# Kernel optimization log

Hardware: AMD Instinct MI355X
Metric: run time of the kernel (lower is better)

The kernel has to match this reference:

```python
import jax, jax.numpy as jnp
import numpy as np

N = 50000        # num_nodes
R = 51           # num_relations
B = 12           # num_bases (hard-coded in module)
D_IN = 64        # initial_size
D_MID = 64       # middle_size
D_OUT2 = 128     # output_size - middle_size - initial_size = 256 - 64 - 64
E = 1600000      # num edges (avg degree 32)


def setup_inputs() -> dict:
    key = jax.random.key(0)
    ks = jax.random.split(key, 11)
    return {
        "edge_index": jax.random.randint(ks[0], (2, E), 0, N),
        "edge_type": jax.random.randint(ks[1], (E,), 0, R),
        "emb": jax.random.normal(ks[2], (N, D_IN)) * 0.1,
        "basis1": jax.random.normal(ks[3], (B, D_IN, D_MID)) * 0.05,
        "comp1": jax.random.normal(ks[4], (R, B)) * 0.3,
        "root1": jax.random.normal(ks[5], (D_IN, D_MID)) * 0.05,
        "bias1": jnp.zeros((D_MID,), jnp.float32),
        "basis2": jax.random.normal(ks[6], (B, D_MID, D_OUT2)) * 0.05,
        "comp2": jax.random.normal(ks[7], (R, B)) * 0.3,
        "root2": jax.random.normal(ks[8], (D_MID, D_OUT2)) * 0.05,
        "bias2": jnp.zeros((D_OUT2,), jnp.float32),
    }


def _rgcn_conv(x, edge_index, edge_type, basis, comp, root, bias):
    """PyG RGCNConv with basis decomposition, per-relation MEAN aggregation,
    root weight and bias. Uses the exact identity
      mean_e(x[src_e] @ W_r) = (mean_e x[src_e]) @ W_r
    to aggregate first (per (node, relation) segment), then transform.
    """
    num_nodes, d_in = x.shape
    src, dst = edge_index[0], edge_index[1]
    seg = dst * R + edge_type                      # combined (node, relation) id
    x_src = x[src]                                 # [E, d_in] gather
    sums = jax.ops.segment_sum(x_src, seg, num_segments=num_nodes * R)
    cnt = jax.ops.segment_sum(jnp.ones((src.shape[0],), x.dtype), seg,
                              num_segments=num_nodes * R)
    agg = (sums / jnp.maximum(cnt, 1.0)[:, None]).reshape(num_nodes, R, d_in)
    W = jnp.einsum('rb,bio->rio', comp, basis)     # [R, d_in, d_out]
    out = jnp.einsum('nri,rio->no', agg, W)        # sum over relations
    return out + x @ root + bias


def reference(edge_index, edge_type, emb, basis1, comp1, root1, bias1,
              basis2, comp2, root2, bias2):
    x1 = jax.nn.relu(_rgcn_conv(emb, edge_index, edge_type, basis1, comp1, root1, bias1))
    x2 = jax.nn.relu(_rgcn_conv(x1, edge_index, edge_type, basis2, comp2, root2, bias2))
    # dropout(p=0.2) is identity in eval mode
    return jnp.concatenate([x2, x1, emb], axis=1)  # [N, 256]
```

## Files before the change

kernel.cpp:

```cpp
#include <hip/hip_runtime.h>
#include <hip/hip_bf16.h>

#define R_REL 51
#define N_BASE 12

typedef __attribute__((ext_vector_type(8))) unsigned short u16x8;
typedef __attribute__((ext_vector_type(8))) short bf16x8;
typedef __attribute__((ext_vector_type(4))) float f32x4;

__device__ __forceinline__ float bf2f(unsigned short u) {
  union { unsigned int i; float f; } c; c.i = ((unsigned int)u) << 16; return c.f;
}
__device__ __forceinline__ unsigned short f2bf(float f) {
  union { float f; unsigned int i; } c; c.f = f;
  return (unsigned short)((c.i + 0x7FFFu + ((c.i >> 16) & 1u)) >> 16);
}

__global__ void k_count(const int* __restrict__ dst, int* __restrict__ cnt, int E) {
  int i = blockIdx.x * 256 + threadIdx.x;
  if (i < E) atomicAdd(&cnt[dst[i]], 1);
}

__global__ void k_scan1(const int* __restrict__ cnt, int* __restrict__ rowptr,
                        int* __restrict__ bsums, int n) {
  __shared__ int s[256];
  int tid = threadIdx.x;
  int i = blockIdx.x * 256 + tid;
  int v = (i < n) ? cnt[i] : 0;
  s[tid] = v;
  __syncthreads();
  for (int off = 1; off < 256; off <<= 1) {
    int t = (tid >= off) ? s[tid - off] : 0;
    __syncthreads();
    s[tid] += t;
    __syncthreads();
  }
  if (i < n) rowptr[i] = s[tid] - v;
  if (tid == 255) bsums[blockIdx.x] = s[255];
}

__global__ void k_scan2(int* __restrict__ bsums, int nb) {
  __shared__ int s[256];
  int tid = threadIdx.x;
  int v = (tid < nb) ? bsums[tid] : 0;
  s[tid] = v;
  __syncthreads();
  for (int off = 1; off < 256; off <<= 1) {
    int t = (tid >= off) ? s[tid - off] : 0;
    __syncthreads();
    s[tid] += t;
    __syncthreads();
  }
  if (tid < nb) bsums[tid] = s[tid] - v;
}

__global__ void k_scan3(int* __restrict__ rowptr, const int* __restrict__ bsums,
                        int n, int E) {
  int i = blockIdx.x * 256 + threadIdx.x;
  if (i < n) rowptr[i] += bsums[blockIdx.x];
  if (blockIdx.x == 0 && threadIdx.x == 0) rowptr[n] = E;
}

__global__ void k_scatter(const int* __restrict__ src, const int* __restrict__ dst,
                          const int* __restrict__ typ, const int* __restrict__ rowptr,
                          int* __restrict__ cursor, unsigned int* __restrict__ edges, int E) {
  int i = blockIdx.x * 256 + threadIdx.x;
  if (i < E) {
    int d = dst[i];
    int pos = rowptr[d] + atomicAdd(&cursor[d], 1);
    edges[pos] = (unsigned int)src[i] | ((unsigned int)typ[i] << 16);
  }
}

__global__ __launch_bounds__(256) void k_agg(
    const float* __restrict__ x,
    int xstride,
    const int* __restrict__ rowptr,
    const unsigned int* __restrict__ edges,
    const float* __restrict__ comp,
    unsigned short* __restrict__ Z,
    int n0, int n1) {
  __shared__ float comp_lds[R_REL * N_BASE];
  __shared__ int   hist[4][64];
  __shared__ float inv[4][64];
  int tid = threadIdx.x;
  for (int idx = tid; idx < R_REL * N_BASE; idx += 256) comp_lds[idx] = comp[idx];
  int wid = tid >> 6, lane = tid & 63;
  if (lane < R_REL) hist[wid][lane] = 0;
  __syncthreads();

  int n = n0 + blockIdx.x * 4 + wid;
  bool valid = (n < n1);
  int e0 = 0, e1 = 0;
  if (valid) { e0 = rowptr[n]; e1 = rowptr[n + 1]; }
  e0 = __builtin_amdgcn_readfirstlane(e0);
  e1 = __builtin_amdgcn_readfirstlane(e1);

  for (int j = e0 + lane; j < e1; j += 64)
    atomicAdd(&hist[wid][edges[j] >> 16], 1);
  __syncthreads();
  if (lane < R_REL) {
    int c = hist[wid][lane];
    inv[wid][lane] = (c > 0) ? (1.0f / (float)c) : 0.0f;
  }
  __syncthreads();

  float z[N_BASE];
#pragma unroll
  for (int b = 0; b < N_BASE; b++) z[b] = 0.0f;

  int j = e0;
  for (; j + 2 <= e1; j += 2) {
    unsigned int eA = edges[j], eB = edges[j + 1];
    int sA = eA & 0xFFFF, rA = eA >> 16;
    int sB = eB & 0xFFFF, rB = eB >> 16;
    float xA = x[(size_t)sA * xstride + lane];
    float xB = x[(size_t)sB * xstride + lane];
    float tA = xA * inv[wid][rA];
    float tB = xB * inv[wid][rB];
    const float* cA = &comp_lds[rA * N_BASE];
    const float* cB = &comp_lds[rB * N_BASE];
#pragma unroll
    for (int b = 0; b < N_BASE; b++) z[b] += tA * cA[b] + tB * cB[b];
  }
  if (j < e1) {
    unsigned int eA = edges[j];
    int sA = eA & 0xFFFF, rA = eA >> 16;
    float xA = x[(size_t)sA * xstride + lane];
    float tA = xA * inv[wid][rA];
    const float* cA = &comp_lds[rA * N_BASE];
#pragma unroll
    for (int b = 0; b < N_BASE; b++) z[b] += tA * cA[b];
  }

  if (valid) {
    size_t base = (size_t)(n - n0) * 832;
#pragma unroll
    for (int b = 0; b < N_BASE; b++)
      Z[base + b * 64 + lane] = f2bf(z[b]);
    Z[base + 768 + lane] = f2bf(x[(size_t)n * xstride + lane]);
  }
}

template <int NOUT>
__global__ void k_prep_w(const float* __restrict__ basis, const float* __restrict__ root,
                         unsigned short* __restrict__ Wf, int total) {
  int idx = blockIdx.x * 256 + threadIdx.x;
  if (idx >= total) return;
  constexpr int NT = NOUT / 16;
  int j = idx & 7;
  int l = (idx >> 3) & 63;
  int t = idx >> 9;
  int nt = t % NT, ks = t / NT;
  int k = ks * 32 + ((l >> 4) * 8) + j;
  int col = nt * 16 + (l & 15);
  float v = (k < 768) ? basis[(size_t)k * NOUT + col]
                      : root[(size_t)(k - 768) * NOUT + col];
  Wf[idx] = f2bf(v);
}

template <int NOUT>
__global__ __launch_bounds__(256) void k_gemm_mfma(
    const unsigned short* __restrict__ Z,
    const unsigned short* __restrict__ Wf,
    const float* __restrict__ bias,
    float* __restrict__ dout,
    int col_off, int n0, int n1) {
  constexpr int NT = NOUT / 16;
  int tid = threadIdx.x;
  int w = tid >> 6, l = tid & 63;
  int m0 = n0 + blockIdx.x * 64 + w * 16;
  int arow = m0 + (l & 15);
  if (arow > n1 - 1) arow = n1 - 1;
  const unsigned short* zp = Z + (size_t)(arow - n0) * 832 + ((l >> 4) * 8);
  const unsigned short* wp = Wf + (size_t)l * 8;

  f32x4 acc[NT];
#pragma unroll
  for (int t = 0; t < NT; t++) acc[t] = (f32x4){0.0f, 0.0f, 0.0f, 0.0f};

  for (int ks = 0; ks < 26; ks++) {
    bf16x8 a = *(const bf16x8*)(zp + ks * 32);
#pragma unroll
    for (int nt = 0; nt < NT; nt++) {
      bf16x8 b = *(const bf16x8*)(wp + (size_t)(ks * NT + nt) * 512);
      acc[nt] = __builtin_amdgcn_mfma_f32_16x16x32_bf16(a, b, acc[nt], 0, 0, 0);
    }
  }

  int rbase = m0 + ((l >> 4) * 4);
  int cl = l & 15;
#pragma unroll
  for (int nt = 0; nt < NT; nt++) {
    int col = col_off + nt * 16 + cl;
    float bv = bias[nt * 16 + cl];
#pragma unroll
    for (int j = 0; j < 4; j++) {
      int row = rbase + j;
      if (row < n1)
        dout[(size_t)row * 256 + col] = fmaxf(acc[nt][j] + bv, 0.0f);
    }
  }
}

__global__ void k_copy_emb(const float* __restrict__ emb, float* __restrict__ dout, int n) {
  int i = blockIdx.x * 256 + threadIdx.x;
  int row = i >> 4, c4 = i & 15;
  if (row < n) {
    float4 v = ((const float4*)emb)[(size_t)row * 16 + c4];
    ((float4*)dout)[(size_t)row * 64 + 48 + c4] = v;
  }
}

extern "C" void kernel_launch(void* const* d_in, const int* in_sizes, int n_in,
                              void* d_out, int out_size, void* d_ws, size_t ws_size,
                              hipStream_t stream) {
  const int*   edge_index = (const int*)d_in[0];
  const int*   edge_type  = (const int*)d_in[1];
  const float* emb        = (const float*)d_in[2];
  const float* basis1     = (const float*)d_in[3];
  const float* comp1      = (const float*)d_in[4];
  const float* root1      = (const float*)d_in[5];
  const float* bias1      = (const float*)d_in[6];
  const float* basis2     = (const float*)d_in[7];
  const float* comp2      = (const float*)d_in[8];
  const float* root2      = (const float*)d_in[9];
  const float* bias2      = (const float*)d_in[10];

  int E = in_sizes[1];
  int N = in_sizes[2] / 64;
  const int* srcp = edge_index;
  const int* dstp = edge_index + E;

  char* ws = (char*)d_ws;
  size_t o = 0;
  auto take = [&](size_t bytes) -> char* {
    char* p = ws + o;
    o += (bytes + 255) & ~(size_t)255;
    return p;
  };
  int*  cnt    = (int*)take((size_t)N * 4);
  int*  rowptr = (int*)take((size_t)(N + 1) * 4);
  int*  bsums  = (int*)take(4096);
  int*  cursor = (int*)take((size_t)N * 4);
  size_t zero_bytes = o;
  unsigned int* edges = (unsigned int*)take((size_t)E * 4);
  constexpr int W1_ELEMS = 26 * 4 * 512;
  constexpr int W2_ELEMS = 26 * 8 * 512;
  unsigned short* Wf1 = (unsigned short*)take((size_t)W1_ELEMS * 2);
  unsigned short* Wf2 = (unsigned short*)take((size_t)W2_ELEMS * 2);
  size_t fixed_end = o;

  size_t avail = (ws_size > fixed_end) ? (ws_size - fixed_end) : 0;
  long long nc = (long long)(avail / (832 * 2));
  if (nc > N) nc = N;
  int nchunk = (int)(nc & ~63LL);
  if (nchunk < 64) nchunk = 64;
  unsigned short* Zb = (unsigned short*)(ws + fixed_end);
  (void)n_in; (void)out_size;

  hipMemsetAsync(d_ws, 0, zero_bytes, stream);

  int nb_e = (E + 255) / 256;
  int nb_n = (N + 255) / 256;
  k_count  <<<nb_e, 256, 0, stream>>>(dstp, cnt, E);
  k_scan1  <<<nb_n, 256, 0, stream>>>(cnt, rowptr, bsums, N);
  k_scan2  <<<1,    256, 0, stream>>>(bsums, nb_n);
  k_scan3  <<<nb_n, 256, 0, stream>>>(rowptr, bsums, N, E);
  k_scatter<<<nb_e, 256, 0, stream>>>(srcp, dstp, edge_type, rowptr, cursor, edges, E);
  k_prep_w<64> <<<(W1_ELEMS + 255) / 256, 256, 0, stream>>>(basis1, root1, Wf1, W1_ELEMS);
  k_prep_w<128><<<(W2_ELEMS + 255) / 256, 256, 0, stream>>>(basis2, root2, Wf2, W2_ELEMS);

  float* dout = (float*)d_out;
  for (int c0 = 0; c0 < N; c0 += nchunk) {
    int c1 = (c0 + nchunk < N) ? c0 + nchunk : N;
    int rows = c1 - c0;
    k_agg<<<(rows + 3) / 4, 256, 0, stream>>>(emb, 64, rowptr, edges, comp1, Zb, c0, c1);
    k_gemm_mfma<64><<<(rows + 63) / 64, 256, 0, stream>>>(Zb, Wf1, bias1, dout, 128, c0, c1);
  }
  for (int c0 = 0; c0 < N; c0 += nchunk) {
    int c1 = (c0 + nchunk < N) ? c0 + nchunk : N;
    int rows = c1 - c0;
    k_agg<<<(rows + 3) / 4, 256, 0, stream>>>(dout + 128, 256, rowptr, edges, comp2, Zb, c0, c1);
    k_gemm_mfma<128><<<(rows + 63) / 64, 256, 0, stream>>>(Zb, Wf2, bias2, dout, 0, c0, c1);
  }
  k_copy_emb<<<(N * 16 + 255) / 256, 256, 0, stream>>>(emb, dout, N);
}
```

Before: 576.8 us.

## Replace global-atomic CSR scatter with two-pass bucketed binning through shared memory

The single-pass edge scatter, which did a global atomic per edge on a per-node cursor and wrote to random positions, is replaced by two passes. The first pass bins edges into 256-node buckets using shared-memory histograms and one global atomic per bucket per block. The second pass scatters each bucket into exact CSR positions using shared-memory atomics. This cuts global atomic traffic and scattered writes at the cost of an extra workspace buffer of E words and one more full pass over the edges. Packing the local node id into the top 8 bits assumes src fits in 16 bits and type in 6 bits. It also relies on N being at most 65536, so the bucket count fits in 256.

```diff
diff --git a/kernel.cpp b/kernel.cpp
--- a/kernel.cpp
+++ b/kernel.cpp
@@ -61,14 +61,61 @@
   if (blockIdx.x == 0 && threadIdx.x == 0) rowptr[n] = E;
 }
 
-__global__ void k_scatter(const int* __restrict__ src, const int* __restrict__ dst,
-                          const int* __restrict__ typ, const int* __restrict__ rowptr,
-                          int* __restrict__ cursor, unsigned int* __restrict__ edges, int E) {
-  int i = blockIdx.x * 256 + threadIdx.x;
-  if (i < E) {
-    int d = dst[i];
-    int pos = rowptr[d] + atomicAdd(&cursor[d], 1);
-    edges[pos] = (unsigned int)src[i] | ((unsigned int)typ[i] << 16);
+__global__ __launch_bounds__(256) void k_binit(const int* __restrict__ rowptr,
+                                               int* __restrict__ bcursor, int N) {
+  int b = threadIdx.x;
+  int n = b << 8; if (n > N) n = N;
+  bcursor[b] = rowptr[n];
+}
+
+__global__ __launch_bounds__(256) void k_bin(
+    const int* __restrict__ src, const int* __restrict__ dst, const int* __restrict__ typ,
+    int* __restrict__ bcursor, unsigned int* __restrict__ binned, int E) {
+  __shared__ int hcnt[256];
+  __shared__ int gbase[256];
+  int tid = threadIdx.x;
+  int base = blockIdx.x * 8192;
+  hcnt[tid] = 0;
+  __syncthreads();
+  for (int q = 0; q < 32; q++) {
+    int idx = base + q * 256 + tid;
+    if (idx < E) atomicAdd(&hcnt[dst[idx] >> 8], 1);
+  }
+  __syncthreads();
+  gbase[tid] = atomicAdd(&bcursor[tid], hcnt[tid]);
+  __syncthreads();
+  hcnt[tid] = 0;
+  __syncthreads();
+  for (int q = 0; q < 32; q++) {
+    int idx = base + q * 256 + tid;
+    if (idx < E) {
+      int d = dst[idx];
+      int bk = d >> 8;
+      unsigned int e = (unsigned int)src[idx] | ((unsigned int)typ[idx] << 16)
+                     | ((unsigned int)(d & 255) << 24);
+      int rank = atomicAdd(&hcnt[bk], 1);
+      binned[gbase[bk] + rank] = e;
+    }
+  }
+}
+
+__global__ __launch_bounds__(256) void k_scatter2(
+    const unsigned int* __restrict__ binned, const int* __restrict__ rowptr,
+    unsigned int* __restrict__ edges, int N) {
+  __shared__ int rp[257];
+  __shared__ int cur[256];
+  int tid = threadIdx.x;
+  int n0 = blockIdx.x << 8;
+  int nn = N - n0; if (nn > 256) nn = 256;
+  for (int i = tid; i <= nn; i += 256) rp[i] = rowptr[n0 + i];
+  cur[tid] = 0;
+  __syncthreads();
+  int e0 = rp[0], e1 = rp[nn];
+  for (int j = e0 + tid; j < e1; j += 256) {
+    unsigned int e = binned[j];
+    int loc = e >> 24;
+    int pos = rp[loc] + atomicAdd(&cur[loc], 1);
+    edges[pos] = e & 0x003FFFFFu;
   }
 }
 
@@ -240,11 +287,12 @@
     return p;
   };
   int*  cnt    = (int*)take((size_t)N * 4);
+  size_t zero_bytes = o;
   int*  rowptr = (int*)take((size_t)(N + 1) * 4);
   int*  bsums  = (int*)take(4096);
-  int*  cursor = (int*)take((size_t)N * 4);
-  size_t zero_bytes = o;
-  unsigned int* edges = (unsigned int*)take((size_t)E * 4);
+  int*  bcursor= (int*)take(256 * 4);
+  unsigned int* binned = (unsigned int*)take((size_t)E * 4);
+  unsigned int* edges  = (unsigned int*)take((size_t)E * 4);
   constexpr int W1_ELEMS = 26 * 4 * 512;
   constexpr int W2_ELEMS = 26 * 8 * 512;
   unsigned short* Wf1 = (unsigned short*)take((size_t)W1_ELEMS * 2);
@@ -263,11 +311,14 @@
 
   int nb_e = (E + 255) / 256;
   int nb_n = (N + 255) / 256;
+  int nbuk = (N + 255) >> 8;
   k_count  <<<nb_e, 256, 0, stream>>>(dstp, cnt, E);
   k_scan1  <<<nb_n, 256, 0, stream>>>(cnt, rowptr, bsums, N);
   k_scan2  <<<1,    256, 0, stream>>>(bsums, nb_n);
   k_scan3  <<<nb_n, 256, 0, stream>>>(rowptr, bsums, N, E);
-  k_scatter<<<nb_e, 256, 0, stream>>>(srcp, dstp, edge_type, rowptr, cursor, edges, E);
+  k_binit  <<<1,    256, 0, stream>>>(rowptr, bcursor, N);
+  k_bin    <<<(E + 8191) / 8192, 256, 0, stream>>>(srcp, dstp, edge_type, bcursor, binned, E);
+  k_scatter2<<<nbuk, 256, 0, stream>>>(binned, rowptr, edges, N);
   k_prep_w<64> <<<(W1_ELEMS + 255) / 256, 256, 0, stream>>>(basis1, root1, Wf1, W1_ELEMS);
   k_prep_w<128><<<(W2_ELEMS + 255) / 256, 256, 0, stream>>>(basis2, root2, Wf2, W2_ELEMS);
 
```

After: 526.6 us. 1.1x faster.
